# Optimization experiments

Hardware: AMD Instinct MI355X
Metric: run time of the kernel (lower is better)

Reference implementation:

```python
import jax, jax.numpy as jnp
import numpy as np

B, R, L_, K_, U_, E = 16, 32, 64, 16, 4, 64  # batch, realizations, APs, users, antennas, embed dim
C2 = 2 * U_                                   # input_dim_2 == output_dim == 2U
EPS = 1e-5


def _uniform(key, shape, fan_out, fan_in):
    # matches torch init: U(-ini, ini) with ini = sqrt(3/(out*in))
    ini = float(np.sqrt(3.0 / (fan_out * fan_in)))
    return jax.random.uniform(key, shape, jnp.float32, -ini, ini)


def setup_inputs() -> dict:
    key = jax.random.key(0)
    ks = jax.random.split(key, 12)
    return {
        "Hhat_real": jax.random.normal(ks[0], (B, R, L_, K_, U_), jnp.float32),
        "Hhat_imag": jax.random.normal(ks[1], (B, R, L_, K_, U_), jnp.float32),
        # layer 0 (hidden, out=E) -- note P3/P5 exist in torch but are unused in forward
        "P1_0": _uniform(ks[2], (E, E), E, E),
        "P2_0": _uniform(ks[3], (E, E), E, E),
        "P4_0": _uniform(ks[4], (E, C2), E, C2),
        "g0": jnp.ones((E,), jnp.float32),
        "b0": jnp.zeros((E,), jnp.float32),
        # layer 1 (hidden, out=E)
        "P1_1": _uniform(ks[5], (E, E), E, E),
        "P2_1": _uniform(ks[6], (E, E), E, E),
        "P4_1": _uniform(ks[7], (E, C2), E, C2),
        "g1": jnp.ones((E,), jnp.float32),
        "b1": jnp.zeros((E,), jnp.float32),
        # layer 2 (output, out=2U, no BN / no ReLU)
        "P1_2": _uniform(ks[8], (C2, E), C2, E),
        "P2_2": _uniform(ks[9], (C2, E), C2, E),
        "P4_2": _uniform(ks[10], (C2, C2), C2, C2),
        "nbrOfRealizations": R,
        "L": L_,
        "K": K_,
        "U": U_,
    }


def _layer(A, H, P1, P2, P4, gamma, beta, is_last):
    # A: [BR, C1, L, K], H: [BR, C2, L, K]
    A1 = jnp.einsum('oc,bclk->bolk', P1, A)
    A2 = jnp.einsum('oc,bcl->bol', P2, A.mean(-1))[:, :, :, None]   # mean over K
    A3 = jnp.einsum('oc,bck->bok', P2, A.mean(-2))[:, :, None, :]   # mean over L
    A4 = jnp.einsum('oc,bcl->bol', P4, H.mean(-1))[:, :, :, None]
    A5 = jnp.einsum('oc,bck->bok', P4, H.mean(-2))[:, :, None, :]
    out = 2 * A1 + 2 * A2 + 2 * A3 + 0.1 * A4 + 0.1 * A5
    if is_last:
        return out
    out = jax.nn.relu(out)
    # BatchNorm2d, training mode: biased variance over (batch, L, K)
    mu = out.mean((0, 2, 3), keepdims=True)
    var = ((out - mu) ** 2).mean((0, 2, 3), keepdims=True)
    return (out - mu) / jnp.sqrt(var + EPS) * gamma[None, :, None, None] + beta[None, :, None, None]


def reference(Hhat_real, Hhat_imag, P1_0, P2_0, P4_0, g0, b0,
              P1_1, P2_1, P4_1, g1, b1, P1_2, P2_2, P4_2,
              nbrOfRealizations, L, K, U):
    batch = Hhat_real.shape[0]
    BR = batch * nbrOfRealizations
    # [B,R,L,K,U] -> [BR,U,L,K] (real / imag channels), concat -> [BR, 2U, L, K]
    Hr = Hhat_real.reshape(BR, L, K, U).transpose(0, 3, 1, 2)
    Hi = Hhat_imag.reshape(BR, L, K, U).transpose(0, 3, 1, 2)
    Hup = jnp.concatenate([Hr, Hi], axis=1)
    A = jnp.zeros((BR, E, L, K), jnp.float32)  # V_AP_updated init
    A = _layer(A, Hup, P1_0, P2_0, P4_0, g0, b0, False)
    A = _layer(A, Hup, P1_1, P2_1, P4_1, g1, b1, False)
    V = _layer(A, Hup, P1_2, P2_2, P4_2, None, None, True)  # [BR, 2U, L, K]
    V = V.reshape(BR, 2, U, L, K)
    F1 = jnp.transpose(V[:, 0], (0, 2, 3, 1))  # [BR, L, K, U]
    F2 = jnp.transpose(V[:, 1], (0, 2, 3, 1))
    norm = jnp.sqrt((F1 ** 2).sum(-1) + (F2 ** 2).sum(-1))[..., None]
    Fhat = (F1 + 1j * F2) / norm
    return Fhat.reshape(batch, nbrOfRealizations, L, K, U)
```

## Files before the change

kernel.cpp:

```cpp
#include <hip/hip_runtime.h>
#include <math.h>

#define BRR 512
#define LLL 64
#define KKK 16
#define EEE 64
#define CC2 8
#define PPP 1024
#define BN_EPS 1e-5f
#define NSTRIPE 16

__device__ __forceinline__ float relu_f(float v){ return v>0.f?v:0.f; }
__device__ __forceinline__ int lds_row(int r){ return r*68 + (((r>>3)&7)<<2); }

#define OFF_HBL  0u
#define OFF_HBK  262144u
#define OFF_Y0   327680u
#define OFF_X1   851968u
#define OFF_Y1   2949120u
#define OFF_X2   3473408u
#define OFF_Y2   3735552u
#define OFF_M1L  3801088u
#define OFF_M1K  5898240u
#define OFF_SUM0 6422528u
#define OFF_SSQ0 6423552u
#define OFF_SUM1 6424576u
#define OFF_SSQ1 6425600u
#define OFF_S0   6426624u
#define OFF_T0   6426688u
#define OFF_S1   6426752u
#define OFF_T1   6426816u
#define WS_FLOATS 6426880u
#define OFF_M1KB 6426880u
#define OFF_T1S  6951168u
#define WS_BIG   40505600u

__global__ void k_zero(float4* __restrict__ p, int n4){
  int t = blockIdx.x*256 + threadIdx.x;
  if (t < n4) p[t] = make_float4(0.f,0.f,0.f,0.f);
}

__global__ __launch_bounds__(256) void k_prep(const float* __restrict__ Hr,
                                              const float* __restrict__ Hi,
                                              const float* __restrict__ P40,
                                              float* __restrict__ ws){
  __shared__ float sm[9344];
  int b = blockIdx.x, tid = threadIdx.x;
  const float* hrg = Hr + (size_t)b*4096;
  const float* hig = Hi + (size_t)b*4096;
  for (int t=tid;t<4096;t+=256){ sm[t]=hrg[t]; sm[4096+t]=hig[t]; }
  for (int t=tid;t<512;t+=256){ int c=t&63,j=t>>6; sm[8192+j*64+c]=P40[c*8+j]; }
  __syncthreads();
  for (int t=tid;t<512;t+=256){ int l=t>>3,c2=t&7;
    const float* src=sm+((c2<4)?0:4096); int u=c2&3;
    float s=0.f;
    #pragma unroll
    for(int k=0;k<16;++k) s+=src[(l*16+k)*4+u];
    sm[8704+t]=s*(1.f/16.f); }
  for (int t=tid;t<128;t+=256){ int k=t>>3,c2=t&7;
    const float* src=sm+((c2<4)?0:4096); int u=c2&3;
    float s=0.f;
    for(int l=0;l<64;++l) s+=src[(l*16+k)*4+u];
    sm[9216+t]=s*(1.f/64.f); }
  __syncthreads();
  for (int t=tid;t<1024;t+=256){ int k=t>>6,c=t&63; float s=0.f;
    #pragma unroll
    for(int j=0;j<8;++j) s+=sm[8192+j*64+c]*sm[9216+k*8+j];
    sm[4096+t]=0.1f*s; }
  for (int t=tid;t<4096;t+=256){ int l=t>>6,c=t&63; float s=0.f;
    #pragma unroll
    for(int j=0;j<8;++j) s+=sm[8192+j*64+c]*sm[8704+l*8+j];
    sm[t]=0.1f*s; }
  __syncthreads();
  for (int t=tid;t<1024;t+=256){ int c=t&63; float yv=sm[4096+t]; float s=0.f;
    for(int l=0;l<64;++l) s+=relu_f(sm[l*64+c]+yv);
    sm[5120+t]=s*(1.f/64.f); }
  float ssum=0.f, ssq=0.f;
  for (int t=tid;t<4096;t+=256){ int c=t&63; float xv=sm[t]; float s=0.f;
    #pragma unroll
    for(int k=0;k<16;++k){ float v=relu_f(xv+sm[4096+k*64+c]); s+=v; ssq+=v*v; }
    ssum+=s;
    ws[OFF_X1+(size_t)b*4096+t]=s*(1.f/16.f); }
  __syncthreads();
  sm[6144+tid]=ssum; sm[6400+tid]=ssq;
  __syncthreads();
  if (tid<64){
    float ts =sm[6144+tid]+sm[6208+tid]+sm[6272+tid]+sm[6336+tid];
    float tss=sm[6400+tid]+sm[6464+tid]+sm[6528+tid]+sm[6592+tid];
    int stripe = b & (NSTRIPE-1);
    atomicAdd(&ws[OFF_SUM0+stripe*64+tid], ts);
    atomicAdd(&ws[OFF_SSQ0+stripe*64+tid], tss);
  }
  for (int t=tid;t<512;t+=256)  ws[OFF_HBL+(size_t)b*512+t]=sm[8704+t];
  for (int t=tid;t<128;t+=256)  ws[OFF_HBK+(size_t)b*128+t]=sm[9216+t];
  for (int t=tid;t<1024;t+=256) ws[OFF_Y0+(size_t)b*1024+t]=sm[4096+t];
  for (int t=tid;t<1024;t+=256) ws[OFF_Y1+(size_t)b*1024+t]=sm[5120+t];
}

__global__ void k_bn(float* __restrict__ ws, const float* __restrict__ g_,
                     const float* __restrict__ b_, unsigned sumOff, unsigned outOff){
  int tid = threadIdx.x;
  if (tid < 64){
    float s=0.f, ss=0.f;
    for (int i=0;i<NSTRIPE;++i){ s+=ws[sumOff+i*64+tid]; ss+=ws[sumOff+1024+i*64+tid]; }
    const float invN = 1.0f/((float)BRR*LLL*KKK);
    float mu=s*invN, var=ss*invN-mu*mu;
    float sc = g_[tid]/sqrtf(var+BN_EPS);
    ws[outOff+tid]=sc;
    ws[outOff+64+tid]=b_[tid]-mu*sc;
  }
}

__global__ __launch_bounds__(256) void k_xy1(float* __restrict__ ws,
                                             const float* __restrict__ P21,
                                             const float* __restrict__ P41){
  __shared__ float wt[4096], p41[512], mrow[1024], hbs[128], s0l[64], t0l[64];
  int bx = blockIdx.x, tid = threadIdx.x;
  for (int t=tid;t<4096;t+=256) wt[t] = 2.0f*P21[(t&63)*64 + (t>>6)];
  for (int t=tid;t<512;t+=256)  p41[t] = P41[t];
  if (tid<64){ s0l[tid]=ws[OFF_S0+tid]; t0l[tid]=ws[OFF_T0+tid]; }
  bool isX = bx < 2048;
  int row0 = isX ? bx*16 : (bx-2048)*16;
  if (isX){
    for (int t=tid;t<1024;t+=256) mrow[t] = ws[OFF_X1+(size_t)row0*64+t];
    if (tid<128) hbs[tid] = ws[OFF_HBL+(size_t)row0*8+tid];
  } else {
    for (int t=tid;t<1024;t+=256) mrow[t] = ws[OFF_Y1+(size_t)row0*64+t];
    if (tid<128) hbs[tid] = ws[OFF_HBK+(size_t)row0*8+tid];
  }
  __syncthreads();
  for (int t=tid;t<1024;t+=256){ int c=t&63; mrow[t]=s0l[c]*mrow[t]+t0l[c]; }
  __syncthreads();
  int r4 = tid>>6, o = tid&63;
  #pragma unroll
  for (int rr=0;rr<4;++rr){
    int rl = rr*4 + r4;
    float s=0.f;
    for (int c=0;c<64;++c) s += wt[c*64+o]*mrow[rl*64+c];
    float s2=0.f;
    #pragma unroll
    for (int j=0;j<8;++j) s2 += p41[o*8+j]*hbs[rl*8+j];
    float res = s + 0.1f*s2;
    if (isX) ws[OFF_X1+(size_t)(row0+rl)*64+o] = res;
    else     ws[OFF_Y1+(size_t)(row0+rl)*64+o] = res;
  }
}

#define T_W1   0
#define T_X08  4384
#define T_Y0   4896
#define T_X1   5984
#define T_Y1   6496
#define T_S0   7520
#define T_T0   7584
#define T_P4T0 7648
#define T_HB8  8160
#define T_END  8224

__device__ void t1_tile(float* sm, const float* __restrict__ ws,
                        const float* __restrict__ P11, const float* __restrict__ P40,
                        int b, int pblk, int tid,
                        float acc[8][4], int og, int pg, int lloc, int c0){
  for (int t=tid;t<4096;t+=256){ int o=t>>6,c=t&63; sm[T_W1+lds_row(o)+c]=2.0f*P11[t]; }
  for (int t=tid;t<1024;t+=256){ int k=t>>6,c=t&63; sm[T_Y0+k*68+c]=ws[OFF_Y0+(size_t)b*1024+t]; }
  for (int t=tid;t<512;t+=256)  sm[T_X1+t]=ws[OFF_X1+((size_t)b*64+pblk*8)*64+t];
  for (int t=tid;t<1024;t+=256) sm[T_Y1+t]=ws[OFF_Y1+(size_t)b*1024+t];
  for (int t=tid;t<512;t+=256){ int c=t&63,j=t>>6; sm[T_P4T0+j*64+c]=P40[c*8+j]; }
  if (tid<64){ sm[T_S0+tid]=ws[OFF_S0+tid]; sm[T_T0+tid]=ws[OFF_T0+tid]; }
  else if (tid<128){ int t2=tid-64; sm[T_HB8+t2]=ws[OFF_HBL+((size_t)b*64+pblk*8)*8+t2]; }
  __syncthreads();
  for (int e=tid;e<512;e+=256){ int l=e>>6,c=e&63; float s=0.f;
    #pragma unroll
    for(int j=0;j<8;++j) s += sm[T_P4T0+j*64+c]*sm[T_HB8+l*8+j];
    sm[T_X08+e]=0.1f*s; }
  __syncthreads();
  {
    float xb[8];
    *(float4*)&xb[0] = *(const float4*)&sm[T_X1 + lloc*64 + c0];
    *(float4*)&xb[4] = *(const float4*)&sm[T_X1 + lloc*64 + c0 + 4];
    #pragma unroll
    for (int i=0;i<4;++i){
      int k=(pg&3)*4+i;
      float yb[8];
      *(float4*)&yb[0] = *(const float4*)&sm[T_Y1 + k*64 + c0];
      *(float4*)&yb[4] = *(const float4*)&sm[T_Y1 + k*64 + c0 + 4];
      #pragma unroll
      for (int j=0;j<8;++j) acc[j][i]=xb[j]+yb[j];
    }
  }
  #pragma unroll 4
  for (int c4=0;c4<16;++c4){
    float4 xr  = *(const float4*)&sm[T_X08 + lloc*64 + c4*4];
    float4 s0v = *(const float4*)&sm[T_S0 + c4*4];
    float4 t0v = *(const float4*)&sm[T_T0 + c4*4];
    float4 aa[4];
    #pragma unroll
    for (int i=0;i<4;++i){
      int k=(pg&3)*4+i;
      float4 yr = *(const float4*)&sm[T_Y0 + k*68 + c4*4];
      aa[i].x = s0v.x*relu_f(xr.x+yr.x)+t0v.x;
      aa[i].y = s0v.y*relu_f(xr.y+yr.y)+t0v.y;
      aa[i].z = s0v.z*relu_f(xr.z+yr.z)+t0v.z;
      aa[i].w = s0v.w*relu_f(xr.w+yr.w)+t0v.w;
    }
    #pragma unroll
    for (int j=0;j<8;++j){
      float4 w = *(const float4*)&sm[T_W1 + lds_row(c0+j) + c4*4];
      #pragma unroll
      for (int i=0;i<4;++i)
        acc[j][i] += w.x*aa[i].x + w.y*aa[i].y + w.z*aa[i].z + w.w*aa[i].w;
    }
  }
  #pragma unroll
  for (int j=0;j<8;++j)
    #pragma unroll
    for (int i=0;i<4;++i) acc[j][i] = relu_f(acc[j][i]);
}

__global__ __launch_bounds__(256) void k_pass1c(float* __restrict__ ws,
                                                const float* __restrict__ P11,
                                                const float* __restrict__ P40){
  __shared__ float sm[8224];
  int b = blockIdx.x >> 1, h = blockIdx.x & 1;
  int pb0 = h*4;
  int tid=threadIdx.x;
  int og=tid&7, pg=tid>>3, lloc=pg>>2, kg=pg&3, c0=og*8, wv=tid>>6;
  for (int t=tid;t<4096;t+=256){ int o=t>>6,c=t&63; sm[T_W1+lds_row(o)+c]=2.0f*P11[t]; }
  for (int t=tid;t<1024;t+=256){ int k=t>>6,c=t&63; sm[T_Y0+k*68+c]=ws[OFF_Y0+(size_t)b*1024+t]; }
  for (int t=tid;t<1024;t+=256) sm[T_Y1+t]=ws[OFF_Y1+(size_t)b*1024+t];
  for (int t=tid;t<512;t+=256){ int c=t&63,j=t>>6; sm[T_P4T0+j*64+c]=P40[c*8+j]; }
  if (tid<64){ sm[T_S0+tid]=ws[OFF_S0+tid]; sm[T_T0+tid]=ws[OFF_T0+tid]; }
  float qsum[8], mk[8][4];
  #pragma unroll
  for (int j=0;j<8;++j){ qsum[j]=0.f;
    #pragma unroll
    for (int i=0;i<4;++i) mk[j][i]=0.f; }
  #pragma unroll 1
  for (int pp=0;pp<4;++pp){
    int pblk = pb0+pp;
    __syncthreads();
    for (int t=tid;t<512;t+=256) sm[T_X1+t]=ws[OFF_X1+((size_t)b*64+pblk*8)*64+t];
    if (tid<64) sm[T_HB8+tid]=ws[OFF_HBL+((size_t)b*64+pblk*8)*8+tid];
    __syncthreads();
    for (int e=tid;e<512;e+=256){ int l=e>>6,c=e&63; float s=0.f;
      #pragma unroll
      for(int j=0;j<8;++j) s += sm[T_P4T0+j*64+c]*sm[T_HB8+l*8+j];
      sm[T_X08+e]=0.1f*s; }
    __syncthreads();
    float acc[8][4];
    {
      float xb[8];
      *(float4*)&xb[0] = *(const float4*)&sm[T_X1 + lloc*64 + c0];
      *(float4*)&xb[4] = *(const float4*)&sm[T_X1 + lloc*64 + c0 + 4];
      #pragma unroll
      for (int i=0;i<4;++i){
        int k=kg*4+i;
        float yb[8];
        *(float4*)&yb[0] = *(const float4*)&sm[T_Y1 + k*64 + c0];
        *(float4*)&yb[4] = *(const float4*)&sm[T_Y1 + k*64 + c0 + 4];
        #pragma unroll
        for (int j=0;j<8;++j) acc[j][i]=xb[j]+yb[j];
      }
    }
    #pragma unroll 4
    for (int c4=0;c4<16;++c4){
      float4 xr  = *(const float4*)&sm[T_X08 + lloc*64 + c4*4];
      float4 s0v = *(const float4*)&sm[T_S0 + c4*4];
      float4 t0v = *(const float4*)&sm[T_T0 + c4*4];
      float4 aa[4];
      #pragma unroll
      for (int i=0;i<4;++i){
        int k=kg*4+i;
        float4 yr = *(const float4*)&sm[T_Y0 + k*68 + c4*4];
        aa[i].x = s0v.x*relu_f(xr.x+yr.x)+t0v.x;
        aa[i].y = s0v.y*relu_f(xr.y+yr.y)+t0v.y;
        aa[i].z = s0v.z*relu_f(xr.z+yr.z)+t0v.z;
        aa[i].w = s0v.w*relu_f(xr.w+yr.w)+t0v.w;
      }
      #pragma unroll
      for (int j=0;j<8;++j){
        float4 w = *(const float4*)&sm[T_W1 + lds_row(c0+j) + c4*4];
        #pragma unroll
        for (int i=0;i<4;++i)
          acc[j][i] += w.x*aa[i].x + w.y*aa[i].y + w.z*aa[i].z + w.w*aa[i].w;
      }
    }
    #pragma unroll
    for (int j=0;j<8;++j)
      #pragma unroll
      for (int i=0;i<4;++i) acc[j][i] = relu_f(acc[j][i]);
    {
      size_t tbase = OFF_T1S + ((size_t)b*8 + pblk)*8192 + (size_t)tid*4;
      #pragma unroll
      for (int j=0;j<8;++j)
        *(float4*)&ws[tbase + j*1024] =
          make_float4(acc[j][0],acc[j][1],acc[j][2],acc[j][3]);
    }
    float sj[8];
    #pragma unroll
    for (int j=0;j<8;++j){
      sj[j]=acc[j][0]+acc[j][1]+acc[j][2]+acc[j][3];
      qsum[j]+=acc[j][0]*acc[j][0]+acc[j][1]*acc[j][1]+acc[j][2]*acc[j][2]+acc[j][3]*acc[j][3];
      #pragma unroll
      for (int i=0;i<4;++i) mk[j][i]+=acc[j][i];
    }
    #pragma unroll
    for (int j=0;j<8;++j){
      float r=sj[j];
      r += __shfl_xor(r, 8, 64);
      r += __shfl_xor(r, 16, 64);
      sj[j]=r;
    }
    if (kg==0){
      const float inv16 = 1.f/16.f;
      float4 v0 = make_float4(sj[0]*inv16, sj[1]*inv16, sj[2]*inv16, sj[3]*inv16);
      float4 v1 = make_float4(sj[4]*inv16, sj[5]*inv16, sj[6]*inv16, sj[7]*inv16);
      size_t base = OFF_M1L + ((size_t)b*64 + pblk*8 + lloc)*64 + c0;
      *(float4*)&ws[base]   = v0;
      *(float4*)&ws[base+4] = v1;
    }
  }
  __syncthreads();
  #pragma unroll
  for (int j=0;j<8;++j){
    #pragma unroll
    for (int i=0;i<4;++i){
      float v = mk[j][i] + __shfl_xor(mk[j][i], 32, 64);
      if ((tid & 32)==0)
        sm[wv*1088 + (og*4+kg)*33 + i*8 + j] = v;
    }
  }
  #pragma unroll
  for (int j=0;j<8;++j) sm[4384+(c0+j)*33+pg] = qsum[j];
  __syncthreads();
  unsigned mko = h ? OFF_M1KB : OFF_M1K;
  float tsacc=0.f;
  #pragma unroll
  for (int r=0;r<4;++r){
    int e = tid + r*256;
    int k=e>>6, c=e&63;
    int a = ((c>>3)*4+(k>>2))*33 + (k&3)*8 + (c&7);
    float v = sm[a]+sm[1088+a]+sm[2176+a]+sm[3264+a];
    tsacc += v;
    ws[mko+(size_t)b*1024+e] = v*(1.f/64.f);
  }
  sm[6496 + (tid&63)*5 + wv] = tsacc;
  __syncthreads();
  if (tid<64){
    float ts  = sm[6496+tid*5+0]+sm[6496+tid*5+1]+sm[6496+tid*5+2]+sm[6496+tid*5+3];
    float tss = 0.f;
    for (int g=0; g<32; ++g) tss += sm[4384+tid*33+g];
    int stripe = b & (NSTRIPE-1);
    atomicAdd(&ws[OFF_SUM1+stripe*64+tid], ts);
    atomicAdd(&ws[OFF_SSQ1+stripe*64+tid], tss);
  }
}

#define MK_OFF 8224
__global__ __launch_bounds__(256) void k_pass1(float* __restrict__ ws,
                                               const float* __restrict__ P11,
                                               const float* __restrict__ P40){
  __shared__ float sm[12576];
  int b=blockIdx.x, tid=threadIdx.x;
  int og=tid&7, pg=tid>>3, lloc=pg>>2, kg=pg&3, c0=og*8, wv=tid>>6;
  for (int t=tid;t<4096;t+=256){ int o=t>>6,c=t&63; sm[T_W1+lds_row(o)+c]=2.0f*P11[t]; }
  for (int t=tid;t<1024;t+=256){ int k=t>>6,c=t&63; sm[T_Y0+k*68+c]=ws[OFF_Y0+(size_t)b*1024+t]; }
  for (int t=tid;t<1024;t+=256) sm[T_Y1+t]=ws[OFF_Y1+(size_t)b*1024+t];
  for (int t=tid;t<512;t+=256){ int c=t&63,j=t>>6; sm[T_P4T0+j*64+c]=P40[c*8+j]; }
  if (tid<64){ sm[T_S0+tid]=ws[OFF_S0+tid]; sm[T_T0+tid]=ws[OFF_T0+tid]; }
  for (int t=tid;t<4352;t+=256) sm[MK_OFF+t]=0.f;
  float qsum[8];
  #pragma unroll
  for (int j=0;j<8;++j) qsum[j]=0.f;
  #pragma unroll 1
  for (int pblk=0;pblk<8;++pblk){
    __syncthreads();
    for (int t=tid;t<512;t+=256) sm[T_X1+t]=ws[OFF_X1+((size_t)b*64+pblk*8)*64+t];
    if (tid<64) sm[T_HB8+tid]=ws[OFF_HBL+((size_t)b*64+pblk*8)*8+tid];
    __syncthreads();
    for (int e=tid;e<512;e+=256){ int l=e>>6,c=e&63; float s=0.f;
      #pragma unroll
      for(int j=0;j<8;++j) s += sm[T_P4T0+j*64+c]*sm[T_HB8+l*8+j];
      sm[T_X08+e]=0.1f*s; }
    __syncthreads();
    float acc[8][4];
    {
      float xb[8];
      *(float4*)&xb[0] = *(const float4*)&sm[T_X1 + lloc*64 + c0];
      *(float4*)&xb[4] = *(const float4*)&sm[T_X1 + lloc*64 + c0 + 4];
      #pragma unroll
      for (int i=0;i<4;++i){
        int k=kg*4+i;
        float yb[8];
        *(float4*)&yb[0] = *(const float4*)&sm[T_Y1 + k*64 + c0];
        *(float4*)&yb[4] = *(const float4*)&sm[T_Y1 + k*64 + c0 + 4];
        #pragma unroll
        for (int j=0;j<8;++j) acc[j][i]=xb[j]+yb[j];
      }
    }
    #pragma unroll 4
    for (int c4=0;c4<16;++c4){
      float4 xr  = *(const float4*)&sm[T_X08 + lloc*64 + c4*4];
      float4 s0v = *(const float4*)&sm[T_S0 + c4*4];
      float4 t0v = *(const float4*)&sm[T_T0 + c4*4];
      float4 aa[4];
      #pragma unroll
      for (int i=0;i<4;++i){
        int k=kg*4+i;
        float4 yr = *(const float4*)&sm[T_Y0 + k*68 + c4*4];
        aa[i].x = s0v.x*relu_f(xr.x+yr.x)+t0v.x;
        aa[i].y = s0v.y*relu_f(xr.y+yr.y)+t0v.y;
        aa[i].z = s0v.z*relu_f(xr.z+yr.z)+t0v.z;
        aa[i].w = s0v.w*relu_f(xr.w+yr.w)+t0v.w;
      }
      #pragma unroll
      for (int j=0;j<8;++j){
        float4 w = *(const float4*)&sm[T_W1 + lds_row(c0+j) + c4*4];
        #pragma unroll
        for (int i=0;i<4;++i)
          acc[j][i] += w.x*aa[i].x + w.y*aa[i].y + w.z*aa[i].z + w.w*aa[i].w;
      }
    }
    #pragma unroll
    for (int j=0;j<8;++j)
      #pragma unroll
      for (int i=0;i<4;++i) acc[j][i] = relu_f(acc[j][i]);
    float sj[8];
    #pragma unroll
    for (int j=0;j<8;++j){
      sj[j]=acc[j][0]+acc[j][1]+acc[j][2]+acc[j][3];
      qsum[j]+=acc[j][0]*acc[j][0]+acc[j][1]*acc[j][1]+acc[j][2]*acc[j][2]+acc[j][3]*acc[j][3];
    }
    #pragma unroll
    for (int j=0;j<8;++j){
      float r=sj[j];
      r += __shfl_xor(r, 8, 64);
      r += __shfl_xor(r, 16, 64);
      sj[j]=r;
    }
    if (kg==0){
      const float inv16 = 1.f/16.f;
      float4 v0 = make_float4(sj[0]*inv16, sj[1]*inv16, sj[2]*inv16, sj[3]*inv16);
      float4 v1 = make_float4(sj[4]*inv16, sj[5]*inv16, sj[6]*inv16, sj[7]*inv16);
      size_t base = OFF_M1L + ((size_t)b*64 + pblk*8 + lloc)*64 + c0;
      *(float4*)&ws[base]   = v0;
      *(float4*)&ws[base+4] = v1;
    }
    #pragma unroll
    for (int j=0;j<8;++j){
      #pragma unroll
      for (int i=0;i<4;++i){
        float v = acc[j][i] + __shfl_xor(acc[j][i], 32, 64);
        if ((tid & 32)==0)
          sm[MK_OFF + wv*1088 + (og*4+kg)*33 + i*8 + j] += v;
      }
    }
  }
  __syncthreads();
  float tsacc=0.f;
  #pragma unroll
  for (int r=0;r<4;++r){
    int e = tid + r*256;
    int k=e>>6, c=e&63;
    int a = ((c>>3)*4+(k>>2))*33 + (k&3)*8 + (c&7);
    float v = sm[MK_OFF+a]+sm[MK_OFF+1088+a]+sm[MK_OFF+2176+a]+sm[MK_OFF+3264+a];
    tsacc += v;
    ws[OFF_M1K+(size_t)b*1024+e] = v*(1.f/64.f);
  }
  __syncthreads();
  sm[8224 + (tid&63)*5 + wv] = tsacc;
  #pragma unroll
  for (int j=0;j<8;++j) sm[8544+(c0+j)*33+pg] = qsum[j];
  __syncthreads();
  if (tid<64){
    float ts  = sm[8224+tid*5+0]+sm[8224+tid*5+1]+sm[8224+tid*5+2]+sm[8224+tid*5+3];
    float tss = 0.f;
    for (int g=0; g<32; ++g) tss += sm[8544+tid*33+g];
    int stripe = b & (NSTRIPE-1);
    atomicAdd(&ws[OFF_SUM1+stripe*64+tid], ts);
    atomicAdd(&ws[OFF_SSQ1+stripe*64+tid], tss);
  }
}

__global__ __launch_bounds__(256) void k_xy2s(float* __restrict__ ws,
                                              const float* __restrict__ P22,
                                              const float* __restrict__ P42,
                                              int two){
  __shared__ float mln[4352];
  __shared__ float mkn[1088];
  __shared__ float w2[512];
  __shared__ float p42s[64];
  __shared__ float hbl[512];
  __shared__ float hbk[128];
  __shared__ float s1l[64], t1l[64];
  int b = blockIdx.x, tid = threadIdx.x;
  if (tid<64){ s1l[tid]=ws[OFF_S1+tid]; t1l[tid]=ws[OFF_T1+tid]; }
  for (int t=tid;t<512;t+=256) w2[t] = 2.0f*P22[(t&7)*64 + (t>>3)];
  if (tid<64) p42s[tid] = P42[tid];
  for (int t=tid;t<512;t+=256) hbl[t] = ws[OFF_HBL+(size_t)b*512+t];
  if (tid<128) hbk[tid] = ws[OFF_HBK+(size_t)b*128+tid];
  __syncthreads();
  for (int t=tid;t<4096;t+=256){ int l=t>>6,c=t&63;
    mln[l*68+c] = s1l[c]*ws[OFF_M1L+(size_t)b*4096+t] + t1l[c]; }
  for (int t=tid;t<1024;t+=256){ int k=t>>6,c=t&63;
    float mv = ws[OFF_M1K+(size_t)b*1024+t];
    if (two) mv += ws[OFF_M1KB+(size_t)b*1024+t];
    mkn[k*68+c] = s1l[c]*mv + t1l[c]; }
  __syncthreads();
  for (int t=tid;t<512;t+=256){
    int l=t>>3, o2=t&7;
    float s=0.f;
    for (int c=0;c<64;++c) s += w2[c*8+o2]*mln[l*68+c];
    float s2=0.f;
    #pragma unroll
    for (int j=0;j<8;++j) s2 += p42s[o2*8+j]*hbl[l*8+j];
    ws[OFF_X2+(size_t)b*512+t] = s + 0.1f*s2;
  }
  if (tid<128){
    int k=tid>>3, o2=tid&7;
    float s=0.f;
    for (int c=0;c<64;++c) s += w2[c*8+o2]*mkn[k*68+c];
    float s2=0.f;
    #pragma unroll
    for (int j=0;j<8;++j) s2 += p42s[o2*8+j]*hbk[k*8+j];
    ws[OFF_Y2+(size_t)b*128+tid] = s + 0.1f*s2;
  }
}

__device__ __forceinline__ void final_epilogue(const float* __restrict__ ws,
                                               float* sm, int b, int pblk, int tid,
                                               float* __restrict__ out,
                                               long long out_cap, int interleaved){
  if (tid < 128){
    int p = tid, k = p & 15, lglob = pblk*8 + (p>>4);
    float a2[8];
    {
      const float* xp = ws + OFF_X2 + ((size_t)b*64+lglob)*8;
      const float* yp = ws + OFF_Y2 + ((size_t)b*16+k)*8;
      float4 x0_ = *(const float4*)&xp[0];
      float4 x1_ = *(const float4*)&xp[4];
      float4 y0_ = *(const float4*)&yp[0];
      float4 y1_ = *(const float4*)&yp[4];
      a2[0]=x0_.x+y0_.x; a2[1]=x0_.y+y0_.y; a2[2]=x0_.z+y0_.z; a2[3]=x0_.w+y0_.w;
      a2[4]=x1_.x+y1_.x; a2[5]=x1_.y+y1_.y; a2[6]=x1_.z+y1_.z; a2[7]=x1_.w+y1_.w;
    }
    for (int c=0;c<64;++c){
      float tn = sm[9028+c]*sm[c*133 + (c>>3) + p] + sm[9092+c];
      #pragma unroll
      for (int o2=0;o2<8;++o2) a2[o2] += sm[8516+o2*64+c]*tn;
    }
    float nrm=0.f;
    #pragma unroll
    for (int o2=0;o2<8;++o2) nrm += a2[o2]*a2[o2];
    float inv = 1.0f/sqrtf(nrm);
    size_t pos = (size_t)b*PPP + lglob*KKK + k;
    if (interleaved){
      long long idx = (long long)pos*8;
      if (idx+8 <= out_cap){
        *(float4*)&out[idx]   = make_float4(a2[0]*inv, a2[4]*inv, a2[1]*inv, a2[5]*inv);
        *(float4*)&out[idx+4] = make_float4(a2[2]*inv, a2[6]*inv, a2[3]*inv, a2[7]*inv);
      }
    } else {
      long long idx = (long long)pos*4;
      if (idx+4 <= out_cap)
        *(float4*)&out[idx] = make_float4(a2[0]*inv, a2[1]*inv, a2[2]*inv, a2[3]*inv);
    }
  }
}

__global__ __launch_bounds__(256) void k_final_big(const float* __restrict__ ws,
                                                   const float* __restrict__ P12,
                                                   float* __restrict__ out,
                                                   long long out_cap, int interleaved){
  __shared__ float sm[9156];
  int bid=blockIdx.x, b=bid>>3, pblk=bid&7, tid=threadIdx.x;
  for (int t=tid;t<512;t+=256) sm[8516+t] = 2.0f*P12[t];
  if (tid<64) sm[9028+tid]=ws[OFF_S1+tid];
  else if (tid<128) sm[9092+(tid-64)]=ws[OFF_T1+(tid-64)];
  {
    size_t base = OFF_T1S + ((size_t)b*8 + pblk)*8192;
    for (int t4=tid;t4<2048;t4+=256){
      float4 v = *(const float4*)&ws[base + (size_t)t4*4];
      int j = t4>>8, lane = t4&255;
      int c = (lane&7)*8 + j;
      int pb = (lane>>5)*16 + ((lane>>3)&3)*4;
      int o = c*133 + (c>>3) + pb;
      sm[o+0]=v.x; sm[o+1]=v.y; sm[o+2]=v.z; sm[o+3]=v.w;
    }
  }
  __syncthreads();
  final_epilogue(ws, sm, b, pblk, tid, out, out_cap, interleaved);
}

__global__ __launch_bounds__(256) void k_final(const float* __restrict__ ws,
                                               const float* __restrict__ P11,
                                               const float* __restrict__ P40,
                                               const float* __restrict__ P12,
                                               float* __restrict__ out,
                                               long long out_cap, int interleaved){
  __shared__ float sm[9156];
  int bid=blockIdx.x, b=bid>>3, pblk=bid&7, tid=threadIdx.x;
  int og=tid&7, pg=tid>>3, lloc=pg>>2, c0=og*8;
  for (int t=tid;t<512;t+=256) sm[8516+t] = 2.0f*P12[t];
  if (tid<64) sm[9028+tid]=ws[OFF_S1+tid];
  else if (tid<128) sm[9092+(tid-64)]=ws[OFF_T1+(tid-64)];
  float acc[8][4];
  t1_tile(sm, ws, P11, P40, b, pblk, tid, acc, og, pg, lloc, c0);
  __syncthreads();
  {
    int kg = pg&3;
    #pragma unroll
    for (int i=0;i<4;++i){
      int p = lloc*16 + kg*4 + i;
      #pragma unroll
      for (int j=0;j<8;++j) sm[(c0+j)*133 + og + p] = acc[j][i];
    }
  }
  __syncthreads();
  final_epilogue(ws, sm, b, pblk, tid, out, out_cap, interleaved);
}

extern "C" void kernel_launch(void* const* d_in, const int* in_sizes, int n_in,
                              void* d_out, int out_size, void* d_ws, size_t ws_size,
                              hipStream_t stream) {
  if (n_in < 15) return;
  if (in_sizes[0] != BRR*4096 || in_sizes[1] != BRR*4096) return;
  if (in_sizes[4] != 512)  return;
  if (in_sizes[7] != 4096) return;
  if (in_sizes[12] != 512) return;
  if (ws_size < (size_t)WS_FLOATS*4) return;

  const float* Hr   = (const float*)d_in[0];
  const float* Hi   = (const float*)d_in[1];
  const float* P4_0 = (const float*)d_in[4];
  const float* g0   = (const float*)d_in[5];
  const float* b0   = (const float*)d_in[6];
  const float* P1_1 = (const float*)d_in[7];
  const float* P2_1 = (const float*)d_in[8];
  const float* P4_1 = (const float*)d_in[9];
  const float* g1   = (const float*)d_in[10];
  const float* b1   = (const float*)d_in[11];
  const float* P1_2 = (const float*)d_in[12];
  const float* P2_2 = (const float*)d_in[13];
  const float* P4_2 = (const float*)d_in[14];
  float* ws  = (float*)d_ws;
  float* out = (float*)d_out;
  int interleaved = (out_size >= 4194304) ? 1 : 0;
  int big = (ws_size >= (size_t)WS_BIG*4) ? 1 : 0;

  k_zero<<<4, 256, 0, stream>>>((float4*)(ws + OFF_SUM0), 4096/4);
  k_prep<<<BRR, 256, 0, stream>>>(Hr, Hi, P4_0, ws);
  k_bn<<<1, 64, 0, stream>>>(ws, g0, b0, OFF_SUM0, OFF_S0);
  k_xy1<<<2560, 256, 0, stream>>>(ws, P2_1, P4_1);
  if (big) k_pass1c<<<BRR*2, 256, 0, stream>>>(ws, P1_1, P4_0);
  else     k_pass1<<<BRR, 256, 0, stream>>>(ws, P1_1, P4_0);
  k_bn<<<1, 64, 0, stream>>>(ws, g1, b1, OFF_SUM1, OFF_S1);
  k_xy2s<<<BRR, 256, 0, stream>>>(ws, P2_2, P4_2, big);
  if (big) k_final_big<<<BRR*8, 256, 0, stream>>>(ws, P1_2, out,
                                                  (long long)out_size, interleaved);
  else     k_final<<<BRR*8, 256, 0, stream>>>(ws, P1_1, P4_0, P1_2, out,
                                              (long long)out_size, interleaved);
}
```

Baseline: 309.8 us.

## Fold BN affine into layer-1 weights, cache X0 term, inline final epilogue

k_prep now writes the per-L layer-0 H-projection tile (sm[0..4096)) to workspace, so pass1 loads it directly instead of recomputing the P4_0·H mean product for each block. The BN0 scale is folded into the layer-1 P1 weights and the shift becomes a precomputed per-output constant, which removes a multiply-add per element from the inner loop. k_final_big replaces the generic epilogue with a two-half split over channels and a shared-memory reduction. This costs extra workspace writes and reads of 4096 floats per batch, plus some setup work per block.

```diff
diff --git a/kernel.cpp b/kernel.cpp
--- a/kernel.cpp
+++ b/kernel.cpp
@@ -95,6 +95,7 @@
   for (int t=tid;t<128;t+=256)  ws[OFF_HBK+(size_t)b*128+t]=sm[9216+t];
   for (int t=tid;t<1024;t+=256) ws[OFF_Y0+(size_t)b*1024+t]=sm[4096+t];
   for (int t=tid;t<1024;t+=256) ws[OFF_Y1+(size_t)b*1024+t]=sm[5120+t];
+  for (int t=tid;t<4096;t+=256) ws[OFF_M1L+(size_t)b*4096+t]=sm[t];
 }
 
 __global__ void k_bn(float* __restrict__ ws, const float* __restrict__ g_,
@@ -153,6 +154,7 @@
 #define T_Y1   6496
 #define T_S0   7520
 #define T_T0   7584
+#define T_CT   7648
 #define T_P4T0 7648
 #define T_HB8  8160
 #define T_END  8224
@@ -217,9 +219,8 @@
     for (int i=0;i<4;++i) acc[j][i] = relu_f(acc[j][i]);
 }
 
-__global__ __launch_bounds__(256) void k_pass1c(float* __restrict__ ws,
-                                                const float* __restrict__ P11,
-                                                const float* __restrict__ P40){
+__global__ __launch_bounds__(256) void k_pass1d(float* __restrict__ ws,
+                                                const float* __restrict__ P11){
   __shared__ float sm[8224];
   int b = blockIdx.x >> 1, h = blockIdx.x & 1;
   int pb0 = h*4;
@@ -228,8 +229,15 @@
   for (int t=tid;t<4096;t+=256){ int o=t>>6,c=t&63; sm[T_W1+lds_row(o)+c]=2.0f*P11[t]; }
   for (int t=tid;t<1024;t+=256){ int k=t>>6,c=t&63; sm[T_Y0+k*68+c]=ws[OFF_Y0+(size_t)b*1024+t]; }
   for (int t=tid;t<1024;t+=256) sm[T_Y1+t]=ws[OFF_Y1+(size_t)b*1024+t];
-  for (int t=tid;t<512;t+=256){ int c=t&63,j=t>>6; sm[T_P4T0+j*64+c]=P40[c*8+j]; }
   if (tid<64){ sm[T_S0+tid]=ws[OFF_S0+tid]; sm[T_T0+tid]=ws[OFF_T0+tid]; }
+  __syncthreads();
+  if (tid<64){
+    float ct=0.f;
+    for (int c=0;c<64;++c) ct += sm[T_W1+lds_row(tid)+c]*sm[T_T0+c];
+    sm[T_CT+tid]=ct;
+  }
+  __syncthreads();
+  for (int t=tid;t<4096;t+=256){ int o=t>>6,c=t&63; sm[T_W1+lds_row(o)+c] *= sm[T_S0+c]; }
   float qsum[8], mk[8][4];
   #pragma unroll
   for (int j=0;j<8;++j){ qsum[j]=0.f;
@@ -240,18 +248,15 @@
     int pblk = pb0+pp;
     __syncthreads();
     for (int t=tid;t<512;t+=256) sm[T_X1+t]=ws[OFF_X1+((size_t)b*64+pblk*8)*64+t];
-    if (tid<64) sm[T_HB8+tid]=ws[OFF_HBL+((size_t)b*64+pblk*8)*8+tid];
-    __syncthreads();
-    for (int e=tid;e<512;e+=256){ int l=e>>6,c=e&63; float s=0.f;
-      #pragma unroll
-      for(int j=0;j<8;++j) s += sm[T_P4T0+j*64+c]*sm[T_HB8+l*8+j];
-      sm[T_X08+e]=0.1f*s; }
+    for (int t=tid;t<512;t+=256) sm[T_X08+t]=ws[OFF_M1L+((size_t)b*64+pblk*8)*64+t];
     __syncthreads();
     float acc[8][4];
     {
-      float xb[8];
-      *(float4*)&xb[0] = *(const float4*)&sm[T_X1 + lloc*64 + c0];
-      *(float4*)&xb[4] = *(const float4*)&sm[T_X1 + lloc*64 + c0 + 4];
+      float xb[8], ctv[8];
+      *(float4*)&xb[0]  = *(const float4*)&sm[T_X1 + lloc*64 + c0];
+      *(float4*)&xb[4]  = *(const float4*)&sm[T_X1 + lloc*64 + c0 + 4];
+      *(float4*)&ctv[0] = *(const float4*)&sm[T_CT + c0];
+      *(float4*)&ctv[4] = *(const float4*)&sm[T_CT + c0 + 4];
       #pragma unroll
       for (int i=0;i<4;++i){
         int k=kg*4+i;
@@ -259,23 +264,21 @@
         *(float4*)&yb[0] = *(const float4*)&sm[T_Y1 + k*64 + c0];
         *(float4*)&yb[4] = *(const float4*)&sm[T_Y1 + k*64 + c0 + 4];
         #pragma unroll
-        for (int j=0;j<8;++j) acc[j][i]=xb[j]+yb[j];
+        for (int j=0;j<8;++j) acc[j][i]=xb[j]+yb[j]+ctv[j];
       }
     }
     #pragma unroll 4
     for (int c4=0;c4<16;++c4){
-      float4 xr  = *(const float4*)&sm[T_X08 + lloc*64 + c4*4];
-      float4 s0v = *(const float4*)&sm[T_S0 + c4*4];
-      float4 t0v = *(const float4*)&sm[T_T0 + c4*4];
+      float4 xr = *(const float4*)&sm[T_X08 + lloc*64 + c4*4];
       float4 aa[4];
       #pragma unroll
       for (int i=0;i<4;++i){
         int k=kg*4+i;
         float4 yr = *(const float4*)&sm[T_Y0 + k*68 + c4*4];
-        aa[i].x = s0v.x*relu_f(xr.x+yr.x)+t0v.x;
-        aa[i].y = s0v.y*relu_f(xr.y+yr.y)+t0v.y;
-        aa[i].z = s0v.z*relu_f(xr.z+yr.z)+t0v.z;
-        aa[i].w = s0v.w*relu_f(xr.w+yr.w)+t0v.w;
+        aa[i].x = relu_f(xr.x+yr.x);
+        aa[i].y = relu_f(xr.y+yr.y);
+        aa[i].z = relu_f(xr.z+yr.z);
+        aa[i].w = relu_f(xr.w+yr.w);
       }
       #pragma unroll
       for (int j=0;j<8;++j){
@@ -589,7 +592,55 @@
     }
   }
   __syncthreads();
-  final_epilogue(ws, sm, b, pblk, tid, out, out_cap, interleaved);
+  int half = tid>>7, p = tid&127;
+  int k = p & 15, lglob = pblk*8 + (p>>4);
+  float a2[8];
+  if (half==0){
+    const float* xp = ws + OFF_X2 + ((size_t)b*64+lglob)*8;
+    const float* yp = ws + OFF_Y2 + ((size_t)b*16+k)*8;
+    float4 x0_ = *(const float4*)&xp[0];
+    float4 x1_ = *(const float4*)&xp[4];
+    float4 y0_ = *(const float4*)&yp[0];
+    float4 y1_ = *(const float4*)&yp[4];
+    a2[0]=x0_.x+y0_.x; a2[1]=x0_.y+y0_.y; a2[2]=x0_.z+y0_.z; a2[3]=x0_.w+y0_.w;
+    a2[4]=x1_.x+y1_.x; a2[5]=x1_.y+y1_.y; a2[6]=x1_.z+y1_.z; a2[7]=x1_.w+y1_.w;
+  } else {
+    #pragma unroll
+    for (int o2=0;o2<8;++o2) a2[o2]=0.f;
+  }
+  int cb = half*32;
+  for (int cc=0;cc<32;++cc){
+    int c = cb+cc;
+    float tn = sm[9028+c]*sm[c*133 + (c>>3) + p] + sm[9092+c];
+    #pragma unroll
+    for (int o2=0;o2<8;++o2) a2[o2] += sm[8516+o2*64+c]*tn;
+  }
+  __syncthreads();
+  if (half==1){
+    #pragma unroll
+    for (int o2=0;o2<8;++o2) sm[p*9+o2] = a2[o2];
+  }
+  __syncthreads();
+  if (half==0){
+    #pragma unroll
+    for (int o2=0;o2<8;++o2) a2[o2] += sm[p*9+o2];
+    float nrm=0.f;
+    #pragma unroll
+    for (int o2=0;o2<8;++o2) nrm += a2[o2]*a2[o2];
+    float inv = 1.0f/sqrtf(nrm);
+    size_t pos = (size_t)b*PPP + lglob*KKK + k;
+    if (interleaved){
+      long long idx = (long long)pos*8;
+      if (idx+8 <= out_cap){
+        *(float4*)&out[idx]   = make_float4(a2[0]*inv, a2[4]*inv, a2[1]*inv, a2[5]*inv);
+        *(float4*)&out[idx+4] = make_float4(a2[2]*inv, a2[6]*inv, a2[3]*inv, a2[7]*inv);
+      }
+    } else {
+      long long idx = (long long)pos*4;
+      if (idx+4 <= out_cap)
+        *(float4*)&out[idx] = make_float4(a2[0]*inv, a2[1]*inv, a2[2]*inv, a2[3]*inv);
+    }
+  }
 }
 
 __global__ __launch_bounds__(256) void k_final(const float* __restrict__ ws,
@@ -652,7 +703,7 @@
   k_prep<<<BRR, 256, 0, stream>>>(Hr, Hi, P4_0, ws);
   k_bn<<<1, 64, 0, stream>>>(ws, g0, b0, OFF_SUM0, OFF_S0);
   k_xy1<<<2560, 256, 0, stream>>>(ws, P2_1, P4_1);
-  if (big) k_pass1c<<<BRR*2, 256, 0, stream>>>(ws, P1_1, P4_0);
+  if (big) k_pass1d<<<BRR*2, 256, 0, stream>>>(ws, P1_1);
   else     k_pass1<<<BRR, 256, 0, stream>>>(ws, P1_1, P4_0);
   k_bn<<<1, 64, 0, stream>>>(ws, g1, b1, OFF_SUM1, OFF_S1);
   k_xy2s<<<BRR, 256, 0, stream>>>(ws, P2_2, P4_2, big);
```

Result: no change. 307.0 us (-0.9%).
